# Kernel tuning notes

Hardware: AMD Instinct MI355X
Metric: run time of the kernel (lower is better)

Reference implementation:

```python
import jax, jax.numpy as jnp
import numpy as np

D_MODEL = 2048
N_HEAD = 16
D_K = D_MODEL // N_HEAD  # 128
B, S = 2, 2048


def setup_inputs() -> dict:
    key = jax.random.key(0)
    ks = jax.random.split(key, 10)
    std = 1.0 / np.sqrt(D_MODEL)
    inp = {
        "x": jax.random.normal(ks[0], (B, S, D_MODEL), dtype=jnp.float32),
        "mask": jnp.ones((B, 1, S, S), dtype=jnp.int32),
        # Linear weights stored as [in, out] for x @ W + b
        "w_q": jax.random.normal(ks[1], (D_MODEL, D_MODEL), dtype=jnp.float32) * std,
        "b_q": jnp.zeros((D_MODEL,), dtype=jnp.float32),
        "w_k": jax.random.normal(ks[2], (D_MODEL, D_K), dtype=jnp.float32) * std,
        "b_k": jnp.zeros((D_K,), dtype=jnp.float32),
        "w_v": jax.random.normal(ks[3], (D_MODEL, D_K), dtype=jnp.float32) * std,
        "b_v": jnp.zeros((D_K,), dtype=jnp.float32),
        "w_o": jax.random.normal(ks[4], (D_MODEL, D_MODEL), dtype=jnp.float32) * std,
        "b_o": jnp.zeros((D_MODEL,), dtype=jnp.float32),
    }
    return inp


def reference(x, mask, w_q, b_q, w_k, b_k, w_v, b_v, w_o, b_o):
    b, s, _ = x.shape
    # Q: [b, h, s, d_k]; K/V single shared head: [b, 1, s, d_k]
    q = (x @ w_q + b_q).reshape(b, s, N_HEAD, D_K).transpose(0, 2, 1, 3)
    k = (x @ w_k + b_k)[:, None, :, :]
    v = (x @ w_v + b_v)[:, None, :, :]
    scale = jnp.sqrt(jnp.float32(D_K))
    # scores: [b, h, s, s] (K head broadcast over h)
    scores = jnp.einsum("bhqd,bzkd->bhqk", q, k) / scale
    scores = jnp.where(mask == 0, jnp.float32(-jnp.inf), scores)
    attn = jax.nn.softmax(scores, axis=-1)
    out = jnp.einsum("bhqk,bzkd->bhqd", attn, v)  # [b, h, s, d_k]
    out = out.transpose(0, 2, 1, 3).reshape(b, s, D_MODEL)
    return out @ w_o + b_o
```

## Files before the change

kernel.cpp:

```cpp
#include <hip/hip_runtime.h>

typedef __attribute__((ext_vector_type(8))) short bf16x8;
typedef __attribute__((ext_vector_type(4))) float f32x4;

#define GLD_LDS16(g, l)                                                        \
  __builtin_amdgcn_global_load_lds(                                            \
      (const __attribute__((address_space(1))) void*)(g),                      \
      (__attribute__((address_space(3))) void*)(l), 16, 0, 0)

__device__ __forceinline__ f32x4 mfma_bf16(bf16x8 a, bf16x8 b, f32x4 c) {
  return __builtin_amdgcn_mfma_f32_16x16x32_bf16(a, b, c, 0, 0, 0);
}

__device__ __forceinline__ unsigned short f2bf(float f) {
  union { float f; unsigned int u; } a;
  a.f = f;
  unsigned int u = a.u;
  unsigned int r = (u + 0x7fffu + ((u >> 16) & 1u)) >> 16;
  return (unsigned short)r;
}


__global__ void k_convert(const float* __restrict__ in,
                          unsigned short* __restrict__ out, int n8) {
  int i = blockIdx.x * 256 + threadIdx.x;
  if (i >= n8) return;
  const float4* p = reinterpret_cast<const float4*>(in) + (size_t)i * 2;
  float4 a = p[0], b = p[1];
  union { unsigned short u[8]; uint4 v; } pk;
  pk.u[0] = f2bf(a.x); pk.u[1] = f2bf(a.y); pk.u[2] = f2bf(a.z); pk.u[3] = f2bf(a.w);
  pk.u[4] = f2bf(b.x); pk.u[5] = f2bf(b.y); pk.u[6] = f2bf(b.z); pk.u[7] = f2bf(b.w);
  reinterpret_cast<uint4*>(out)[i] = pk.v;
}

__global__ void k_transpose(const float* __restrict__ in,
                            unsigned short* __restrict__ out, int R, int C) {
  __shared__ float tile[32][33];
  int c0 = blockIdx.x * 32, r0 = blockIdx.y * 32;
  int tx = threadIdx.x, ty = threadIdx.y;
#pragma unroll
  for (int j = 0; j < 4; ++j)
    tile[ty + j * 8][tx] = in[(size_t)(r0 + ty + j * 8) * C + (c0 + tx)];
  __syncthreads();
#pragma unroll
  for (int j = 0; j < 4; ++j)
    out[(size_t)(c0 + ty + j * 8) * R + (r0 + tx)] = f2bf(tile[tx][ty + j * 8]);
}

__global__ void k_transpose_v(const unsigned short* __restrict__ qkv,
                              unsigned short* __restrict__ vT) {
  __shared__ unsigned short tile[32][33];
  int k0 = blockIdx.x * 32, d0 = blockIdx.y * 32, b = blockIdx.z;
  int tx = threadIdx.x, ty = threadIdx.y;
  const unsigned short* src = qkv + ((size_t)b * 2048 + k0) * 2304 + 2176 + d0;
#pragma unroll
  for (int j = 0; j < 4; ++j)
    tile[ty + j * 8][tx] = src[(size_t)(ty + j * 8) * 2304 + tx];
  __syncthreads();
#pragma unroll
  for (int j = 0; j < 4; ++j) {
    int d = d0 + ty + j * 8;
    int k = k0 + tx;
    int ks = (k & ~63) | (((((k >> 3) & 7) ^ (d & 7)) << 3)) | (k & 7);
    vT[(size_t)b * 262144 + (size_t)d * 2048 + ks] = tile[tx][ty + j * 8];
  }
}

__global__ void k_bias_concat(const float* __restrict__ bq,
                              const float* __restrict__ bk,
                              const float* __restrict__ bv,
                              float* __restrict__ o) {
  int i = blockIdx.x * 256 + threadIdx.x;
  if (i < 2048) o[i] = bq[i];
  else if (i < 2176) o[i] = bk[i - 2048];
  else if (i < 2304) o[i] = bv[i - 2176];
}


template <bool OUT_F32>
__global__ __launch_bounds__(256, 2) void k_gemm(
    const unsigned short* __restrict__ A, const unsigned short* __restrict__ Bt,
    const float* __restrict__ bias, void* __restrict__ Cp, int M, int N, int K) {
  __shared__ __align__(16) unsigned short lda[2][128 * 32];
  __shared__ __align__(16) unsigned short ldb[2][128 * 32];
  const int t = threadIdx.x;
  const int l = t & 63;
  const int w = t >> 6;
  const int wr = w >> 1, wc = w & 1;
  const int lr = l & 15, lg = l >> 4;
  const int m0 = blockIdx.y * 128, n0 = blockIdx.x * 128;

  f32x4 acc[4][4] = {};

#pragma unroll
  for (int c = 0; c < 2; ++c) {
    int idx = t * 8 + c * 2048;
    int row = idx >> 5, col = idx & 31;
    GLD_LDS16(A + (size_t)(m0 + row) * K + col, &lda[0][0] + w * 512 + c * 2048);
    GLD_LDS16(Bt + (size_t)(n0 + row) * K + col, &ldb[0][0] + w * 512 + c * 2048);
  }
  __syncthreads();

  int cur = 0;
  for (int kt = 32; kt < K; kt += 32) {
#pragma unroll
    for (int c = 0; c < 2; ++c) {
      int idx = t * 8 + c * 2048;
      int row = idx >> 5, col = idx & 31;
      GLD_LDS16(A + (size_t)(m0 + row) * K + kt + col,
                &lda[cur ^ 1][0] + w * 512 + c * 2048);
      GLD_LDS16(Bt + (size_t)(n0 + row) * K + kt + col,
                &ldb[cur ^ 1][0] + w * 512 + c * 2048);
    }
    bf16x8 af[4], bfr[4];
#pragma unroll
    for (int i = 0; i < 4; ++i)
      af[i] = *reinterpret_cast<const bf16x8*>(&lda[cur][0] + (wr * 64 + i * 16 + lr) * 32 + lg * 8);
#pragma unroll
    for (int j = 0; j < 4; ++j)
      bfr[j] = *reinterpret_cast<const bf16x8*>(&ldb[cur][0] + (wc * 64 + j * 16 + lr) * 32 + lg * 8);
#pragma unroll
    for (int i = 0; i < 4; ++i)
#pragma unroll
      for (int j = 0; j < 4; ++j)
        acc[i][j] = mfma_bf16(af[i], bfr[j], acc[i][j]);
    __syncthreads();
    cur ^= 1;
  }
  {
    bf16x8 af[4], bfr[4];
#pragma unroll
    for (int i = 0; i < 4; ++i)
      af[i] = *reinterpret_cast<const bf16x8*>(&lda[cur][0] + (wr * 64 + i * 16 + lr) * 32 + lg * 8);
#pragma unroll
    for (int j = 0; j < 4; ++j)
      bfr[j] = *reinterpret_cast<const bf16x8*>(&ldb[cur][0] + (wc * 64 + j * 16 + lr) * 32 + lg * 8);
#pragma unroll
    for (int i = 0; i < 4; ++i)
#pragma unroll
      for (int j = 0; j < 4; ++j)
        acc[i][j] = mfma_bf16(af[i], bfr[j], acc[i][j]);
  }

#pragma unroll
  for (int j = 0; j < 4; ++j) {
    int col = n0 + wc * 64 + j * 16 + lr;
    float bv = bias[col];
#pragma unroll
    for (int i = 0; i < 4; ++i) {
      int rowb = m0 + wr * 64 + i * 16 + lg * 4;
#pragma unroll
      for (int r = 0; r < 4; ++r) {
        float v = acc[i][j][r] + bv;
        if (OUT_F32)
          reinterpret_cast<float*>(Cp)[(size_t)(rowb + r) * N + col] = v;
        else
          reinterpret_cast<unsigned short*>(Cp)[(size_t)(rowb + r) * N + col] = f2bf(v);
      }
    }
  }
}


__global__ __launch_bounds__(512, 4) void k_attn(
    const unsigned short* __restrict__ qkv,
    const unsigned short* __restrict__ vT,
    unsigned short* __restrict__ out) {
  __shared__ __align__(16) unsigned short k_lds[2][64 * 128];
  __shared__ __align__(16) unsigned short v_lds[2][128 * 64];
  __shared__ __align__(16) unsigned short p_lds[128 * 64];

  const int t = threadIdx.x, l = t & 63, w = t >> 6;
  const int lr = l & 15, lg = l >> 4;
  const int bid = blockIdx.x;
  const int qt = bid & 15, h = (bid >> 4) & 15, b = bid >> 8;
  const size_t rowQ0 = (size_t)b * 2048 + qt * 128;
  const size_t rowK0 = (size_t)b * 2048;
  const unsigned short* vTb = vT + (size_t)b * 262144;

  bf16x8 qf[4];
  {
    const unsigned short* qrow = qkv + (rowQ0 + w * 16 + lr) * 2304 + h * 128;
#pragma unroll
    for (int kd = 0; kd < 4; ++kd)
      qf[kd] = *reinterpret_cast<const bf16x8*>(qrow + kd * 32 + lg * 8);
  }

#pragma unroll
  for (int c = 0; c < 2; ++c) {
    int f16 = t + c * 512;
    int row = f16 >> 4;
    int col16 = (f16 & 15) ^ (row & 7);
    GLD_LDS16(qkv + (rowK0 + row) * 2304 + 2048 + col16 * 8,
              &k_lds[0][0] + w * 512 + c * 4096);
  }
#pragma unroll
  for (int c = 0; c < 2; ++c) {
    int unit = t + c * 512;
    int d = unit >> 3, u = unit & 7;
    GLD_LDS16(vTb + (size_t)d * 2048 + u * 8,
              &v_lds[0][0] + w * 512 + c * 4096);
  }
  __syncthreads();

  f32x4 o_acc[8] = {};
  float m_s = -1e30f, l_s = 0.f;

  const float C_SM = 0.08838834764831845f * 1.4426950408889634f;

  for (int kc = 0; kc < 32; ++kc) {
    const int cur = kc & 1;
    const unsigned short* kl = &k_lds[cur][0];
    const unsigned short* vl = &v_lds[cur][0];

    if (kc < 31) {
#pragma unroll
      for (int c = 0; c < 2; ++c) {
        int f16 = t + c * 512;
        int row = f16 >> 4;
        int col16 = (f16 & 15) ^ (row & 7);
        GLD_LDS16(qkv + (rowK0 + (kc + 1) * 64 + row) * 2304 + 2048 + col16 * 8,
                  &k_lds[cur ^ 1][0] + w * 512 + c * 4096);
      }
#pragma unroll
      for (int c = 0; c < 2; ++c) {
        int unit = t + c * 512;
        int d = unit >> 3, u = unit & 7;
        GLD_LDS16(vTb + (size_t)d * 2048 + (kc + 1) * 64 + u * 8,
                  &v_lds[cur ^ 1][0] + w * 512 + c * 4096);
      }
    }

    f32x4 sf[4];
    __builtin_amdgcn_s_setprio(1);
#pragma unroll
    for (int ctK = 0; ctK < 4; ++ctK) {
      f32x4 s = {0.f, 0.f, 0.f, 0.f};
#pragma unroll
      for (int kd = 0; kd < 4; ++kd) {
        int row = ctK * 16 + lr;
        int u = (kd * 4 + lg) ^ (row & 7);
        bf16x8 kf = *reinterpret_cast<const bf16x8*>(kl + row * 128 + u * 8);
        s = mfma_bf16(kf, qf[kd], s);
      }
      sf[ctK] = s;
    }
    __builtin_amdgcn_s_setprio(0);

    float vmax;
    {
      f32x4 m4 = sf[0];
#pragma unroll
      for (int ctK = 1; ctK < 4; ++ctK) {
        m4[0] = fmaxf(m4[0], sf[ctK][0]); m4[1] = fmaxf(m4[1], sf[ctK][1]);
        m4[2] = fmaxf(m4[2], sf[ctK][2]); m4[3] = fmaxf(m4[3], sf[ctK][3]);
      }
      vmax = fmaxf(fmaxf(m4[0], m4[1]), fmaxf(m4[2], m4[3]));
      vmax = fmaxf(vmax, __shfl_xor(vmax, 16));
      vmax = fmaxf(vmax, __shfl_xor(vmax, 32));
    }
    if (!__all(vmax <= m_s)) {
      float newm = fmaxf(m_s, vmax);
      float alpha = __builtin_amdgcn_exp2f((m_s - newm) * C_SM);
      m_s = newm;
      l_s *= alpha;
#pragma unroll
      for (int r = 0; r < 4; ++r) {
        float a_r = __shfl(alpha, lg * 4 + r);
#pragma unroll
        for (int ct8 = 0; ct8 < 8; ++ct8) o_acc[ct8][r] *= a_r;
      }
    }
    {
      float psum = 0.f;
#pragma unroll
      for (int ctK = 0; ctK < 4; ++ctK) {
#pragma unroll
        for (int r = 0; r < 4; ++r) {
          float p = __builtin_amdgcn_exp2f((sf[ctK][r] - m_s) * C_SM);
          sf[ctK][r] = p;
          psum += p;
        }
      }
      psum += __shfl_xor(psum, 16);
      psum += __shfl_xor(psum, 32);
      l_s += psum;
    }

#pragma unroll
    for (int ctK = 0; ctK < 4; ++ctK) {
      union { unsigned short u[4]; uint2 v; } pk;
#pragma unroll
      for (int r = 0; r < 4; ++r) pk.u[r] = f2bf(sf[ctK][r]);
      *reinterpret_cast<uint2*>(
          p_lds + (w * 16 + lr) * 64 + ((ctK * 16 + lg * 4) ^ ((lr & 7) << 3))) = pk.v;
    }

    __builtin_amdgcn_s_setprio(1);
#pragma unroll
    for (int ks = 0; ks < 2; ++ks) {
      bf16x8 pf = *reinterpret_cast<const bf16x8*>(
          p_lds + (w * 16 + lr) * 64 + ((ks * 32 + lg * 8) ^ ((lr & 7) << 3)));
#pragma unroll
      for (int ct8 = 0; ct8 < 8; ++ct8) {
        bf16x8 vf = *reinterpret_cast<const bf16x8*>(
            vl + (ct8 * 16 + lr) * 64 + (((ks * 4 + lg) ^ (lr & 7)) * 8));
        o_acc[ct8] = mfma_bf16(pf, vf, o_acc[ct8]);
      }
    }
    __builtin_amdgcn_s_setprio(0);

    __syncthreads();
  }

  float inv = 1.0f / l_s;
  float inv4[4];
#pragma unroll
  for (int r = 0; r < 4; ++r) inv4[r] = __shfl(inv, lg * 4 + r);
#pragma unroll
  for (int r = 0; r < 4; ++r) {
    size_t row = rowQ0 + w * 16 + lg * 4 + r;
#pragma unroll
    for (int ct8 = 0; ct8 < 8; ++ct8)
      out[row * 2048 + h * 128 + ct8 * 16 + lr] = f2bf(o_acc[ct8][r] * inv4[r]);
  }
}


extern "C" void kernel_launch(void* const* d_in, const int* in_sizes, int n_in,
                              void* d_out, int out_size, void* d_ws,
                              size_t ws_size, hipStream_t stream) {
  const float* x  = (const float*)d_in[0];
  const float* wq = (const float*)d_in[2];
  const float* bq = (const float*)d_in[3];
  const float* wk = (const float*)d_in[4];
  const float* bk = (const float*)d_in[5];
  const float* wv = (const float*)d_in[6];
  const float* bv = (const float*)d_in[7];
  const float* wo = (const float*)d_in[8];
  const float* bo = (const float*)d_in[9];
  float* out = (float*)d_out;

  char* ws = (char*)d_ws;
  unsigned short* xb    = (unsigned short*)(ws);
  unsigned short* wqkvT = (unsigned short*)(ws + 16777216);
  unsigned short* woT   = (unsigned short*)(ws + 26214400);
  unsigned short* qkvb  = (unsigned short*)(ws + 34603008);
  float*          biasq = (float*)(ws + 53477376);
  unsigned short* vTb   = (unsigned short*)(ws + 53486592);

  k_convert<<<4096, 256, 0, stream>>>(x, xb, 1048576);
  k_transpose<<<dim3(64, 64), dim3(32, 8), 0, stream>>>(wq, wqkvT, 2048, 2048);
  k_transpose<<<dim3(4, 64),  dim3(32, 8), 0, stream>>>(wk, wqkvT + (size_t)2048 * 2048, 2048, 128);
  k_transpose<<<dim3(4, 64),  dim3(32, 8), 0, stream>>>(wv, wqkvT + (size_t)2176 * 2048, 2048, 128);
  k_transpose<<<dim3(64, 64), dim3(32, 8), 0, stream>>>(wo, woT, 2048, 2048);
  k_bias_concat<<<9, 256, 0, stream>>>(bq, bk, bv, biasq);

  k_gemm<false><<<dim3(18, 32), 256, 0, stream>>>(xb, wqkvT, biasq, qkvb, 4096, 2304, 2048);
  k_transpose_v<<<dim3(64, 4, 2), dim3(32, 8), 0, stream>>>(qkvb, vTb);
  k_attn<<<512, 512, 0, stream>>>(qkvb, vTb, xb);
  k_gemm<true><<<dim3(16, 32), 256, 0, stream>>>(xb, woT, bo, out, 4096, 2048, 2048);
}
```

Before: 362.8 us.

## Deepen GEMM LDS pipeline to four stages, swizzle tile order, use packed bf16 convert

The projection GEMM moves from a double-buffered LDS pipeline to a four-buffer ring with three tiles in flight. Explicit vmcnt waits replace the full __syncthreads per k-step, which is meant to hide global-load latency better. Workgroup indices are remapped by a stride-8 swizzle to change which tiles run together and improve L2 reuse. Separately, the attention kernel's softmax-probability conversion to bf16 now uses the hardware v_cvt_pk_bf16_f32 instruction instead of software rounding. The cost is double the GEMM LDS footprint (64KB per block), which may limit the intended two blocks per CU.

New measurement: 385.9 us. 1.06x slower.

```diff
diff --git a/kernel.cpp b/kernel.cpp
--- a/kernel.cpp
+++ b/kernel.cpp
@@ -18,6 +18,12 @@
   unsigned int u = a.u;
   unsigned int r = (u + 0x7fffu + ((u >> 16) & 1u)) >> 16;
   return (unsigned short)r;
+}
+
+__device__ __forceinline__ unsigned cvt_pk_bf16(float lo, float hi) {
+  unsigned r;
+  asm volatile("v_cvt_pk_bf16_f32 %0, %1, %2" : "=v"(r) : "v"(lo), "v"(hi));
+  return r;
 }
 
 
@@ -81,66 +87,69 @@
 __global__ __launch_bounds__(256, 2) void k_gemm(
     const unsigned short* __restrict__ A, const unsigned short* __restrict__ Bt,
     const float* __restrict__ bias, void* __restrict__ Cp, int M, int N, int K) {
-  __shared__ __align__(16) unsigned short lda[2][128 * 32];
-  __shared__ __align__(16) unsigned short ldb[2][128 * 32];
+  __shared__ __align__(16) unsigned short lda[4][128 * 32];
+  __shared__ __align__(16) unsigned short ldb[4][128 * 32];
   const int t = threadIdx.x;
   const int l = t & 63;
   const int w = t >> 6;
   const int wr = w >> 1, wc = w & 1;
   const int lr = l & 15, lg = l >> 4;
-  const int m0 = blockIdx.y * 128, n0 = blockIdx.x * 128;
+
+  int gx = gridDim.x;
+  int nwg = gx * gridDim.y;
+  int lin = blockIdx.y * gx + blockIdx.x;
+  int swz = (lin & 7) * (nwg >> 3) + (lin >> 3);
+  const int m0 = (swz / gx) * 128, n0 = (swz % gx) * 128;
+
+  const int srow0 = t >> 2, scol = (t & 3) * 8;
+  const size_t aBase = (size_t)(m0 + srow0) * K + scol;
+  const size_t a2Base = (size_t)(m0 + srow0 + 64) * K + scol;
+  const size_t bBase = (size_t)(n0 + srow0) * K + scol;
+  const size_t b2Base = (size_t)(n0 + srow0 + 64) * K + scol;
+  const int ldsOff = w * 512;
 
   f32x4 acc[4][4] = {};
 
-#pragma unroll
-  for (int c = 0; c < 2; ++c) {
-    int idx = t * 8 + c * 2048;
-    int row = idx >> 5, col = idx & 31;
-    GLD_LDS16(A + (size_t)(m0 + row) * K + col, &lda[0][0] + w * 512 + c * 2048);
-    GLD_LDS16(Bt + (size_t)(n0 + row) * K + col, &ldb[0][0] + w * 512 + c * 2048);
-  }
-  __syncthreads();
-
-  int cur = 0;
-  for (int kt = 32; kt < K; kt += 32) {
-#pragma unroll
-    for (int c = 0; c < 2; ++c) {
-      int idx = t * 8 + c * 2048;
-      int row = idx >> 5, col = idx & 31;
-      GLD_LDS16(A + (size_t)(m0 + row) * K + kt + col,
-                &lda[cur ^ 1][0] + w * 512 + c * 2048);
-      GLD_LDS16(Bt + (size_t)(n0 + row) * K + kt + col,
-                &ldb[cur ^ 1][0] + w * 512 + c * 2048);
-    }
+#define STAGE_G(buf, kt)                                                       \
+  do {                                                                         \
+    GLD_LDS16(A + aBase + (kt), &lda[buf][0] + ldsOff);                        \
+    GLD_LDS16(A + a2Base + (kt), &lda[buf][0] + 2048 + ldsOff);                \
+    GLD_LDS16(Bt + bBase + (kt), &ldb[buf][0] + ldsOff);                       \
+    GLD_LDS16(Bt + b2Base + (kt), &ldb[buf][0] + 2048 + ldsOff);               \
+  } while (0)
+
+  const int nsteps = K >> 5;
+  STAGE_G(0, 0);
+  STAGE_G(1, 32);
+  STAGE_G(2, 64);
+
+  for (int i = 0; i < nsteps; ++i) {
+    if (i < nsteps - 2)
+      asm volatile("s_waitcnt vmcnt(8)" ::: "memory");
+    else if (i == nsteps - 2)
+      asm volatile("s_waitcnt vmcnt(4)" ::: "memory");
+    else
+      asm volatile("s_waitcnt vmcnt(0)" ::: "memory");
+    __builtin_amdgcn_s_barrier();
+
+    if (i + 3 < nsteps) STAGE_G((i + 3) & 3, (i + 3) * 32);
+
+    const unsigned short* la = &lda[i & 3][0];
+    const unsigned short* lb = &ldb[i & 3][0];
     bf16x8 af[4], bfr[4];
 #pragma unroll
-    for (int i = 0; i < 4; ++i)
-      af[i] = *reinterpret_cast<const bf16x8*>(&lda[cur][0] + (wr * 64 + i * 16 + lr) * 32 + lg * 8);
+    for (int ii = 0; ii < 4; ++ii)
+      af[ii] = *reinterpret_cast<const bf16x8*>(la + (wr * 64 + ii * 16 + lr) * 32 + lg * 8);
 #pragma unroll
     for (int j = 0; j < 4; ++j)
-      bfr[j] = *reinterpret_cast<const bf16x8*>(&ldb[cur][0] + (wc * 64 + j * 16 + lr) * 32 + lg * 8);
-#pragma unroll
-    for (int i = 0; i < 4; ++i)
+      bfr[j] = *reinterpret_cast<const bf16x8*>(lb + (wc * 64 + j * 16 + lr) * 32 + lg * 8);
+#pragma unroll
+    for (int ii = 0; ii < 4; ++ii)
 #pragma unroll
       for (int j = 0; j < 4; ++j)
-        acc[i][j] = mfma_bf16(af[i], bfr[j], acc[i][j]);
-    __syncthreads();
-    cur ^= 1;
-  }
-  {
-    bf16x8 af[4], bfr[4];
-#pragma unroll
-    for (int i = 0; i < 4; ++i)
-      af[i] = *reinterpret_cast<const bf16x8*>(&lda[cur][0] + (wr * 64 + i * 16 + lr) * 32 + lg * 8);
-#pragma unroll
-    for (int j = 0; j < 4; ++j)
-      bfr[j] = *reinterpret_cast<const bf16x8*>(&ldb[cur][0] + (wc * 64 + j * 16 + lr) * 32 + lg * 8);
-#pragma unroll
-    for (int i = 0; i < 4; ++i)
-#pragma unroll
-      for (int j = 0; j < 4; ++j)
-        acc[i][j] = mfma_bf16(af[i], bfr[j], acc[i][j]);
-  }
+        acc[ii][j] = mfma_bf16(af[ii], bfr[j], acc[ii][j]);
+  }
+#undef STAGE_G
 
 #pragma unroll
   for (int j = 0; j < 4; ++j) {
@@ -289,11 +298,11 @@
 
 #pragma unroll
     for (int ctK = 0; ctK < 4; ++ctK) {
-      union { unsigned short u[4]; uint2 v; } pk;
-#pragma unroll
-      for (int r = 0; r < 4; ++r) pk.u[r] = f2bf(sf[ctK][r]);
+      uint2 pk;
+      pk.x = cvt_pk_bf16(sf[ctK][0], sf[ctK][1]);
+      pk.y = cvt_pk_bf16(sf[ctK][2], sf[ctK][3]);
       *reinterpret_cast<uint2*>(
-          p_lds + (w * 16 + lr) * 64 + ((ctK * 16 + lg * 4) ^ ((lr & 7) << 3))) = pk.v;
+          p_lds + (w * 16 + lr) * 64 + ((ctK * 16 + lg * 4) ^ ((lr & 7) << 3))) = pk;
     }
 
     __builtin_amdgcn_s_setprio(1);
```

## Retile GEMM to 128x64 with workgroup swizzle and double attention query rows per block

Applied to the files above, without the earlier changes.

The GEMM tile shrinks from 128x128 to 128x64, doubling the block count, and uses an XCD-style workgroup swizzle with higher occupancy bounds. The attention kernel now processes 256 query rows per block, two 16-row tiles per wave, so each K/V LDS tile is reused across twice as many queries. The P conversion to bf16 now uses a packed hardware convert instruction. Together these aim to improve GEMM load balance and cut attention K/V reloads, at the cost of more registers in attention and only 256 attention blocks.

Result: slower. 374.1 us (+3.1%).

```diff
diff --git a/kernel.cpp b/kernel.cpp
--- a/kernel.cpp
+++ b/kernel.cpp
@@ -18,6 +18,12 @@
   unsigned int u = a.u;
   unsigned int r = (u + 0x7fffu + ((u >> 16) & 1u)) >> 16;
   return (unsigned short)r;
+}
+
+__device__ __forceinline__ unsigned cvt_pk_bf16(float lo, float hi) {
+  unsigned r;
+  asm volatile("v_cvt_pk_bf16_f32 %0, %1, %2" : "=v"(r) : "v"(lo), "v"(hi));
+  return r;
 }
 
 
@@ -78,73 +84,78 @@
 
 
 template <bool OUT_F32>
-__global__ __launch_bounds__(256, 2) void k_gemm(
+__global__ __launch_bounds__(256, 4) void k_gemm(
     const unsigned short* __restrict__ A, const unsigned short* __restrict__ Bt,
     const float* __restrict__ bias, void* __restrict__ Cp, int M, int N, int K) {
   __shared__ __align__(16) unsigned short lda[2][128 * 32];
-  __shared__ __align__(16) unsigned short ldb[2][128 * 32];
+  __shared__ __align__(16) unsigned short ldb[2][64 * 32];
   const int t = threadIdx.x;
   const int l = t & 63;
   const int w = t >> 6;
   const int wr = w >> 1, wc = w & 1;
   const int lr = l & 15, lg = l >> 4;
-  const int m0 = blockIdx.y * 128, n0 = blockIdx.x * 128;
-
-  f32x4 acc[4][4] = {};
-
-#pragma unroll
-  for (int c = 0; c < 2; ++c) {
-    int idx = t * 8 + c * 2048;
-    int row = idx >> 5, col = idx & 31;
-    GLD_LDS16(A + (size_t)(m0 + row) * K + col, &lda[0][0] + w * 512 + c * 2048);
-    GLD_LDS16(Bt + (size_t)(n0 + row) * K + col, &ldb[0][0] + w * 512 + c * 2048);
-  }
+
+  int gx = gridDim.x;
+  int nwg = gx * gridDim.y;
+  int lin = blockIdx.y * gx + blockIdx.x;
+  int swz = (lin & 7) * (nwg >> 3) + (lin >> 3);
+  const int m0 = (swz / gx) * 128, n0 = (swz % gx) * 64;
+
+  const int srow0 = t >> 2, scol = (t & 3) * 8;
+  const size_t aBase = (size_t)(m0 + srow0) * K + scol;
+  const size_t a2Base = (size_t)(m0 + srow0 + 64) * K + scol;
+  const size_t bBase = (size_t)(n0 + srow0) * K + scol;
+  const int ldsOff = w * 512;
+
+  f32x4 acc[4][2] = {};
+
+#define STAGE_G(buf, kt)                                                       \
+  do {                                                                         \
+    GLD_LDS16(A + aBase + (kt), &lda[buf][0] + ldsOff);                        \
+    GLD_LDS16(A + a2Base + (kt), &lda[buf][0] + 2048 + ldsOff);                \
+    GLD_LDS16(Bt + bBase + (kt), &ldb[buf][0] + ldsOff);                       \
+  } while (0)
+
+  STAGE_G(0, 0);
   __syncthreads();
 
   int cur = 0;
   for (int kt = 32; kt < K; kt += 32) {
-#pragma unroll
-    for (int c = 0; c < 2; ++c) {
-      int idx = t * 8 + c * 2048;
-      int row = idx >> 5, col = idx & 31;
-      GLD_LDS16(A + (size_t)(m0 + row) * K + kt + col,
-                &lda[cur ^ 1][0] + w * 512 + c * 2048);
-      GLD_LDS16(Bt + (size_t)(n0 + row) * K + kt + col,
-                &ldb[cur ^ 1][0] + w * 512 + c * 2048);
-    }
-    bf16x8 af[4], bfr[4];
+    STAGE_G(cur ^ 1, kt);
+    bf16x8 af[4], bfr[2];
 #pragma unroll
     for (int i = 0; i < 4; ++i)
       af[i] = *reinterpret_cast<const bf16x8*>(&lda[cur][0] + (wr * 64 + i * 16 + lr) * 32 + lg * 8);
 #pragma unroll
-    for (int j = 0; j < 4; ++j)
-      bfr[j] = *reinterpret_cast<const bf16x8*>(&ldb[cur][0] + (wc * 64 + j * 16 + lr) * 32 + lg * 8);
+    for (int j = 0; j < 2; ++j)
+      bfr[j] = *reinterpret_cast<const bf16x8*>(&ldb[cur][0] + (wc * 32 + j * 16 + lr) * 32 + lg * 8);
 #pragma unroll
     for (int i = 0; i < 4; ++i)
 #pragma unroll
-      for (int j = 0; j < 4; ++j)
+      for (int j = 0; j < 2; ++j)
         acc[i][j] = mfma_bf16(af[i], bfr[j], acc[i][j]);
     __syncthreads();
     cur ^= 1;
   }
   {
-    bf16x8 af[4], bfr[4];
+    bf16x8 af[4], bfr[2];
 #pragma unroll
     for (int i = 0; i < 4; ++i)
       af[i] = *reinterpret_cast<const bf16x8*>(&lda[cur][0] + (wr * 64 + i * 16 + lr) * 32 + lg * 8);
 #pragma unroll
-    for (int j = 0; j < 4; ++j)
-      bfr[j] = *reinterpret_cast<const bf16x8*>(&ldb[cur][0] + (wc * 64 + j * 16 + lr) * 32 + lg * 8);
+    for (int j = 0; j < 2; ++j)
+      bfr[j] = *reinterpret_cast<const bf16x8*>(&ldb[cur][0] + (wc * 32 + j * 16 + lr) * 32 + lg * 8);
 #pragma unroll
     for (int i = 0; i < 4; ++i)
 #pragma unroll
-      for (int j = 0; j < 4; ++j)
+      for (int j = 0; j < 2; ++j)
         acc[i][j] = mfma_bf16(af[i], bfr[j], acc[i][j]);
   }
-
-#pragma unroll
-  for (int j = 0; j < 4; ++j) {
-    int col = n0 + wc * 64 + j * 16 + lr;
+#undef STAGE_G
+
+#pragma unroll
+  for (int j = 0; j < 2; ++j) {
+    int col = n0 + wc * 32 + j * 16 + lr;
     float bv = bias[col];
 #pragma unroll
     for (int i = 0; i < 4; ++i) {
@@ -162,28 +173,30 @@
 }
 
 
-__global__ __launch_bounds__(512, 4) void k_attn(
+__global__ __launch_bounds__(512, 2) void k_attn(
     const unsigned short* __restrict__ qkv,
     const unsigned short* __restrict__ vT,
     unsigned short* __restrict__ out) {
   __shared__ __align__(16) unsigned short k_lds[2][64 * 128];
   __shared__ __align__(16) unsigned short v_lds[2][128 * 64];
-  __shared__ __align__(16) unsigned short p_lds[128 * 64];
+  __shared__ __align__(16) unsigned short p_lds[256 * 64];
 
   const int t = threadIdx.x, l = t & 63, w = t >> 6;
   const int lr = l & 15, lg = l >> 4;
   const int bid = blockIdx.x;
-  const int qt = bid & 15, h = (bid >> 4) & 15, b = bid >> 8;
-  const size_t rowQ0 = (size_t)b * 2048 + qt * 128;
+  const int qt = bid & 7, h = (bid >> 3) & 15, b = bid >> 7;
+  const size_t rowQ0 = (size_t)b * 2048 + qt * 256;
   const size_t rowK0 = (size_t)b * 2048;
   const unsigned short* vTb = vT + (size_t)b * 262144;
 
-  bf16x8 qf[4];
-  {
-    const unsigned short* qrow = qkv + (rowQ0 + w * 16 + lr) * 2304 + h * 128;
+  bf16x8 qf[2][4];
+#pragma unroll
+  for (int rt = 0; rt < 2; ++rt) {
+    const unsigned short* qrow =
+        qkv + (rowQ0 + w * 32 + rt * 16 + lr) * 2304 + h * 128;
 #pragma unroll
     for (int kd = 0; kd < 4; ++kd)
-      qf[kd] = *reinterpret_cast<const bf16x8*>(qrow + kd * 32 + lg * 8);
+      qf[rt][kd] = *reinterpret_cast<const bf16x8*>(qrow + kd * 32 + lg * 8);
   }
 
 #pragma unroll
@@ -203,8 +216,8 @@
   }
   __syncthreads();
 
-  f32x4 o_acc[8] = {};
-  float m_s = -1e30f, l_s = 0.f;
+  f32x4 o_acc[2][8] = {};
+  float m_s[2] = {-1e30f, -1e30f}, l_s[2] = {0.f, 0.f};
 
   const float C_SM = 0.08838834764831845f * 1.4426950408889634f;
 
@@ -231,81 +244,88 @@
       }
     }
 
-    f32x4 sf[4];
+    f32x4 sf[2][4];
     __builtin_amdgcn_s_setprio(1);
 #pragma unroll
     for (int ctK = 0; ctK < 4; ++ctK) {
-      f32x4 s = {0.f, 0.f, 0.f, 0.f};
+      f32x4 s0 = {0.f, 0.f, 0.f, 0.f}, s1 = {0.f, 0.f, 0.f, 0.f};
 #pragma unroll
       for (int kd = 0; kd < 4; ++kd) {
         int row = ctK * 16 + lr;
         int u = (kd * 4 + lg) ^ (row & 7);
         bf16x8 kf = *reinterpret_cast<const bf16x8*>(kl + row * 128 + u * 8);
-        s = mfma_bf16(kf, qf[kd], s);
-      }
-      sf[ctK] = s;
+        s0 = mfma_bf16(kf, qf[0][kd], s0);
+        s1 = mfma_bf16(kf, qf[1][kd], s1);
+      }
+      sf[0][ctK] = s0; sf[1][ctK] = s1;
     }
     __builtin_amdgcn_s_setprio(0);
 
-    float vmax;
-    {
-      f32x4 m4 = sf[0];
-#pragma unroll
-      for (int ctK = 1; ctK < 4; ++ctK) {
-        m4[0] = fmaxf(m4[0], sf[ctK][0]); m4[1] = fmaxf(m4[1], sf[ctK][1]);
-        m4[2] = fmaxf(m4[2], sf[ctK][2]); m4[3] = fmaxf(m4[3], sf[ctK][3]);
-      }
-      vmax = fmaxf(fmaxf(m4[0], m4[1]), fmaxf(m4[2], m4[3]));
-      vmax = fmaxf(vmax, __shfl_xor(vmax, 16));
-      vmax = fmaxf(vmax, __shfl_xor(vmax, 32));
-    }
-    if (!__all(vmax <= m_s)) {
-      float newm = fmaxf(m_s, vmax);
-      float alpha = __builtin_amdgcn_exp2f((m_s - newm) * C_SM);
-      m_s = newm;
-      l_s *= alpha;
-#pragma unroll
-      for (int r = 0; r < 4; ++r) {
-        float a_r = __shfl(alpha, lg * 4 + r);
-#pragma unroll
-        for (int ct8 = 0; ct8 < 8; ++ct8) o_acc[ct8][r] *= a_r;
-      }
-    }
-    {
-      float psum = 0.f;
+#pragma unroll
+    for (int rt = 0; rt < 2; ++rt) {
+      float vmax;
+      {
+        f32x4 m4 = sf[rt][0];
+#pragma unroll
+        for (int ctK = 1; ctK < 4; ++ctK) {
+          m4[0] = fmaxf(m4[0], sf[rt][ctK][0]); m4[1] = fmaxf(m4[1], sf[rt][ctK][1]);
+          m4[2] = fmaxf(m4[2], sf[rt][ctK][2]); m4[3] = fmaxf(m4[3], sf[rt][ctK][3]);
+        }
+        vmax = fmaxf(fmaxf(m4[0], m4[1]), fmaxf(m4[2], m4[3]));
+        vmax = fmaxf(vmax, __shfl_xor(vmax, 16));
+        vmax = fmaxf(vmax, __shfl_xor(vmax, 32));
+      }
+      if (!__all(vmax <= m_s[rt])) {
+        float newm = fmaxf(m_s[rt], vmax);
+        float alpha = __builtin_amdgcn_exp2f((m_s[rt] - newm) * C_SM);
+        m_s[rt] = newm;
+        l_s[rt] *= alpha;
+#pragma unroll
+        for (int r = 0; r < 4; ++r) {
+          float a_r = __shfl(alpha, lg * 4 + r);
+#pragma unroll
+          for (int ct8 = 0; ct8 < 8; ++ct8) o_acc[rt][ct8][r] *= a_r;
+        }
+      }
+      {
+        float psum = 0.f;
+#pragma unroll
+        for (int ctK = 0; ctK < 4; ++ctK) {
+#pragma unroll
+          for (int r = 0; r < 4; ++r) {
+            float p = __builtin_amdgcn_exp2f((sf[rt][ctK][r] - m_s[rt]) * C_SM);
+            sf[rt][ctK][r] = p;
+            psum += p;
+          }
+        }
+        psum += __shfl_xor(psum, 16);
+        psum += __shfl_xor(psum, 32);
+        l_s[rt] += psum;
+      }
 #pragma unroll
       for (int ctK = 0; ctK < 4; ++ctK) {
-#pragma unroll
-        for (int r = 0; r < 4; ++r) {
-          float p = __builtin_amdgcn_exp2f((sf[ctK][r] - m_s) * C_SM);
-          sf[ctK][r] = p;
-          psum += p;
-        }
-      }
-      psum += __shfl_xor(psum, 16);
-      psum += __shfl_xor(psum, 32);
-      l_s += psum;
-    }
-
-#pragma unroll
-    for (int ctK = 0; ctK < 4; ++ctK) {
-      union { unsigned short u[4]; uint2 v; } pk;
-#pragma unroll
-      for (int r = 0; r < 4; ++r) pk.u[r] = f2bf(sf[ctK][r]);
-      *reinterpret_cast<uint2*>(
-          p_lds + (w * 16 + lr) * 64 + ((ctK * 16 + lg * 4) ^ ((lr & 7) << 3))) = pk.v;
+        uint2 pk;
+        pk.x = cvt_pk_bf16(sf[rt][ctK][0], sf[rt][ctK][1]);
+        pk.y = cvt_pk_bf16(sf[rt][ctK][2], sf[rt][ctK][3]);
+        *reinterpret_cast<uint2*>(
+            p_lds + (w * 32 + rt * 16 + lr) * 64 +
+            ((ctK * 16 + lg * 4) ^ ((lr & 7) << 3))) = pk;
+      }
     }
 
     __builtin_amdgcn_s_setprio(1);
 #pragma unroll
     for (int ks = 0; ks < 2; ++ks) {
-      bf16x8 pf = *reinterpret_cast<const bf16x8*>(
-          p_lds + (w * 16 + lr) * 64 + ((ks * 32 + lg * 8) ^ ((lr & 7) << 3)));
+      bf16x8 pf0 = *reinterpret_cast<const bf16x8*>(
+          p_lds + (w * 32 + lr) * 64 + ((ks * 32 + lg * 8) ^ ((lr & 7) << 3)));
+      bf16x8 pf1 = *reinterpret_cast<const bf16x8*>(
+          p_lds + (w * 32 + 16 + lr) * 64 + ((ks * 32 + lg * 8) ^ ((lr & 7) << 3)));
 #pragma unroll
       for (int ct8 = 0; ct8 < 8; ++ct8) {
         bf16x8 vf = *reinterpret_cast<const bf16x8*>(
             vl + (ct8 * 16 + lr) * 64 + (((ks * 4 + lg) ^ (lr & 7)) * 8));
-        o_acc[ct8] = mfma_bf16(pf, vf, o_acc[ct8]);
+        o_acc[0][ct8] = mfma_bf16(pf0, vf, o_acc[0][ct8]);
+        o_acc[1][ct8] = mfma_bf16(pf1, vf, o_acc[1][ct8]);
       }
     }
     __builtin_amdgcn_s_setprio(0);
@@ -313,16 +333,19 @@
     __syncthreads();
   }
 
-  float inv = 1.0f / l_s;
-  float inv4[4];
-#pragma unroll
-  for (int r = 0; r < 4; ++r) inv4[r] = __shfl(inv, lg * 4 + r);
-#pragma unroll
-  for (int r = 0; r < 4; ++r) {
-    size_t row = rowQ0 + w * 16 + lg * 4 + r;
-#pragma unroll
-    for (int ct8 = 0; ct8 < 8; ++ct8)
-      out[row * 2048 + h * 128 + ct8 * 16 + lr] = f2bf(o_acc[ct8][r] * inv4[r]);
+#pragma unroll
+  for (int rt = 0; rt < 2; ++rt) {
+    float inv = 1.0f / l_s[rt];
+    float inv4[4];
+#pragma unroll
+    for (int r = 0; r < 4; ++r) inv4[r] = __shfl(inv, lg * 4 + r);
+#pragma unroll
+    for (int r = 0; r < 4; ++r) {
+      size_t row = rowQ0 + w * 32 + rt * 16 + lg * 4 + r;
+#pragma unroll
+      for (int ct8 = 0; ct8 < 8; ++ct8)
+        out[row * 2048 + h * 128 + ct8 * 16 + lr] = f2bf(o_acc[rt][ct8][r] * inv4[r]);
+    }
   }
 }
 
@@ -356,8 +379,8 @@
   k_transpose<<<dim3(64, 64), dim3(32, 8), 0, stream>>>(wo, woT, 2048, 2048);
   k_bias_concat<<<9, 256, 0, stream>>>(bq, bk, bv, biasq);
 
-  k_gemm<false><<<dim3(18, 32), 256, 0, stream>>>(xb, wqkvT, biasq, qkvb, 4096, 2304, 2048);
+  k_gemm<false><<<dim3(36, 32), 256, 0, stream>>>(xb, wqkvT, biasq, qkvb, 4096, 2304, 2048);
   k_transpose_v<<<dim3(64, 4, 2), dim3(32, 8), 0, stream>>>(qkvb, vTb);
-  k_attn<<<512, 512, 0, stream>>>(qkvb, vTb, xb);
-  k_gemm<true><<<dim3(16, 32), 256, 0, stream>>>(xb, woT, bo, out, 4096, 2048, 2048);
-}
+  k_attn<<<256, 512, 0, stream>>>(qkvb, vTb, xb);
+  k_gemm<true><<<dim3(32, 32), 256, 0, stream>>>(xb, woT, bo, out, 4096, 2048, 2048);
+}
```
